# Performance work log

Measured on AMD Instinct MI355X. Metric: run time of the kernel, lower is better.

The kernel has to match this reference:

```python
import jax, jax.numpy as jnp
import numpy as np

EMBED_DIM = 1024
N_HEADS = 16

def setup_inputs() -> dict:
    key = jax.random.key(0)
    k1, k2, k3 = jax.random.split(key, 3)
    x = jax.random.normal(k1, (4, 2048, EMBED_DIM), dtype=jnp.float32)
    # nn.Linear(D, 3D): store weight as [D, 3D] for x @ W
    W_qkv = jax.random.normal(k2, (EMBED_DIM, 3 * EMBED_DIM), dtype=jnp.float32) * (1.0 / np.sqrt(EMBED_DIM))
    b_qkv = jax.random.normal(k3, (3 * EMBED_DIM,), dtype=jnp.float32) * 0.02
    return {"x": x, "W_qkv": W_qkv, "b_qkv": b_qkv}

def reference(x, W_qkv, b_qkv):
    bs, T, D = x.shape
    nh = N_HEADS
    hs = D // nh
    # fused qkv projection -> [bs, T, nh, 3, hs] (matches view(bs,T,nh,3*hs) + split(hs))
    qkv = (jnp.einsum('btd,de->bte', x, W_qkv) + b_qkv).reshape(bs, T, nh, 3, hs)
    q = qkv[..., 0, :].transpose(0, 2, 1, 3)  # [bs, nh, T, hs]
    k = qkv[..., 1, :].transpose(0, 2, 1, 3)
    v = qkv[..., 2, :].transpose(0, 2, 1, 3)
    scale = 1.0 / np.sqrt(hs).astype(np.float32)
    scores = jnp.einsum('bhqd,bhkd->bhqk', q, k) * scale  # [bs, nh, T, T]
    attn = jax.nn.softmax(scores, axis=-1)
    out = jnp.einsum('bhqk,bhkd->bhqd', attn, v)  # [bs, nh, T, hs]
    return out.transpose(0, 2, 1, 3).reshape(bs, T, D)
```

## Files before the change

kernel.cpp:

```cpp
#include <hip/hip_runtime.h>
#include <stdint.h>

#define T_SEQ 2048
#define DMODEL 1024
#define NHEAD 16
#define HS 64
#define N3 3072
#define BSZ 4
#define MTOT (BSZ*T_SEQ)

typedef __attribute__((ext_vector_type(8))) short bf16x8;
typedef __attribute__((ext_vector_type(4))) float f32x4;
typedef __attribute__((ext_vector_type(16))) float f32x16;
typedef __attribute__((ext_vector_type(2))) unsigned int uint2v;

#define QSCALE 0.18033688011112042f
#define SM_SHIFT 12.0f

#define BH_STRIDE 131072

__device__ inline unsigned short f2bf(float f){
  union { float f; uint32_t u; } v; v.f = f;
  uint32_t r = (v.u + 0x7fffu + ((v.u >> 16) & 1u)) >> 16;
  return (unsigned short)r;
}

__device__ inline uint32_t cvtpk_bf16(float lo, float hi){
  uint32_t r;
  asm("v_cvt_pk_bf16_f32 %0, %1, %2" : "=v"(r) : "v"(lo), "v"(hi));
  return r;
}

__device__ inline void plswap(uint32_t &a, uint32_t &b){
  uint2v r = __builtin_amdgcn_permlane32_swap(a, b, false, false);
  a = r[0]; b = r[1];
}

__device__ inline void gld16(const void* g, void* l){
  __builtin_amdgcn_global_load_lds((const __attribute__((address_space(1))) void*)g,
                                   (__attribute__((address_space(3))) void*)l, 16, 0, 0);
}

__global__ __launch_bounds__(256) void cvt_x(const float* __restrict__ x,
                                             unsigned short* __restrict__ xb, int n){
  int stride = gridDim.x * blockDim.x;
  for (int i = blockIdx.x * blockDim.x + threadIdx.x; i * 4 < n; i += stride){
    const float4 v = *(const float4*)(x + (size_t)i * 4);
    ushort4 o; o.x = f2bf(v.x); o.y = f2bf(v.y); o.z = f2bf(v.z); o.w = f2bf(v.w);
    *(ushort4*)(xb + (size_t)i * 4) = o;
  }
}

__global__ __launch_bounds__(256) void cvt_wt(const float* __restrict__ W,
                                              unsigned short* __restrict__ Wt){
  __shared__ float tile[32][33];
  int bx = blockIdx.x;
  int by = blockIdx.y;
  int tx = threadIdx.x;
  int ty = threadIdx.y;
#pragma unroll
  for (int i = 0; i < 4; i++){
    int k = by * 32 + ty + i * 8;
    int n = bx * 32 + tx;
    tile[ty + i * 8][tx] = W[(size_t)k * N3 + n];
  }
  __syncthreads();
#pragma unroll
  for (int i = 0; i < 4; i++){
    int n = bx * 32 + ty + i * 8;
    int k = by * 32 + tx;
    Wt[(size_t)n * DMODEL + k] = f2bf(tile[tx][ty + i * 8]);
  }
}

#define BM 128
#define BN 128
#define BK 32

__global__ __launch_bounds__(256, 2) void gemm_qkv(
    const unsigned short* __restrict__ xb, const unsigned short* __restrict__ wt,
    const float* __restrict__ bias,
    unsigned short* __restrict__ Qb, unsigned short* __restrict__ Kb,
    unsigned short* __restrict__ Vt)
{
  __shared__ unsigned short Al[BM * BK];
  __shared__ unsigned short Bl[BN * BK];
  const int tid = threadIdx.x;
  const int lane = tid & 63;
  const int w  = tid >> 6;
  const int wm = w >> 1, wn = w & 1;
  const int lr = lane & 15, lg = lane >> 4;
  const int m0 = blockIdx.x * BM;
  const int n0 = blockIdx.y * BN;

  f32x4 acc[4][4] = {};

  const int srow = tid >> 2;
  const int scol = (tid & 3) * 8;
  const unsigned short* ga0 = xb + (size_t)(m0 + srow) * DMODEL + scol;
  const unsigned short* gb0 = wt + (size_t)(n0 + srow) * DMODEL + scol;
  unsigned short* la = &Al[tid * 8];
  unsigned short* lb = &Bl[tid * 8];

  for (int k0 = 0; k0 < DMODEL; k0 += BK){
    gld16(ga0 + k0, la);
    gld16(ga0 + k0 + (size_t)64 * DMODEL, la + 2048);
    gld16(gb0 + k0, lb);
    gld16(gb0 + k0 + (size_t)64 * DMODEL, lb + 2048);
    __syncthreads();
    bf16x8 af[4], bfg[4];
#pragma unroll
    for (int i = 0; i < 4; i++){
      af[i]  = *(const bf16x8*)&Al[(wm * 64 + i * 16 + lr) * BK + lg * 8];
      bfg[i] = *(const bf16x8*)&Bl[(wn * 64 + i * 16 + lr) * BK + lg * 8];
    }
#pragma unroll
    for (int i = 0; i < 4; i++)
#pragma unroll
      for (int j = 0; j < 4; j++)
        acc[i][j] = __builtin_amdgcn_mfma_f32_16x16x32_bf16(af[i], bfg[j], acc[i][j], 0, 0, 0);
    __syncthreads();
  }

#pragma unroll
  for (int i = 0; i < 4; i++){
#pragma unroll
    for (int j = 0; j < 4; j++){
      int gn = n0 + wn * 64 + j * 16 + lr;
      float bv = bias[gn];
      int h = gn / 192;
      int rem = gn - h * 192;
      int which = rem >> 6;
      int d = rem & 63;
#pragma unroll
      for (int r = 0; r < 4; r++){
        int gm = m0 + wm * 64 + i * 16 + lg * 4 + r;
        int b = gm >> 11, t = gm & 2047;
        float val = acc[i][j][r] + bv;
        size_t base = (size_t)(b * NHEAD + h) * BH_STRIDE + (size_t)(t >> 5) * 2048;
        if (which == 0)
          Qb[base + (d >> 4) * 512 + ((d >> 3) & 1) * 256 + (t & 31) * 8 + (d & 7)] = f2bf(val * QSCALE);
        else if (which == 1)
          Kb[base + (d >> 4) * 512 + ((d >> 3) & 1) * 256 + (t & 31) * 8 + (d & 7)] = f2bf(val);
        else {
          int kv = t & 31;
          Vt[base + (d >> 5) * 1024 + (kv >> 4) * 512 + ((kv >> 3) & 1) * 256 + (d & 31) * 8 + (kv & 7)] = f2bf(val);
        }
      }
    }
  }
}

__global__ __launch_bounds__(256, 3) void attn(
    const unsigned short* __restrict__ Qb, const unsigned short* __restrict__ Kb,
    const unsigned short* __restrict__ Vt, float* __restrict__ out)
{
  __shared__ unsigned short KVs[2][2][2][2048];

  int flat = blockIdx.x + (blockIdx.y << 4) + (blockIdx.z << 8);
  int wid = (flat & 7) * 128 + (flat >> 3);
  const int bx = wid & 15;
  const int h  = (wid >> 4) & 15;
  const int b  = wid >> 8;

  const int tid = threadIdx.x;
  const int lane = tid & 63;
  const int w = tid >> 6;
  const int ql = lane & 31;
  const int hi = lane >> 5;
  const int bh = b * NHEAD + h;
  const int q0 = bx * 128 + w * 32;

  const unsigned short* Qf = Qb + (size_t)bh * BH_STRIDE;
  const unsigned short* Kg = Kb + (size_t)bh * BH_STRIDE;
  const unsigned short* Vg = Vt + (size_t)bh * BH_STRIDE;

  bf16x8 qf[4];
#pragma unroll
  for (int c = 0; c < 4; c++)
    qf[c] = *(const bf16x8*)(Qf + (size_t)(q0 >> 5) * 2048 + c * 512 + lane * 8);

  f32x16 cinit;
#pragma unroll
  for (int r = 0; r < 16; r++) cinit[r] = -SM_SHIFT;

  f32x16 acc0 = {}, acc1 = {};
  float lA = 0.f, lB = 0.f, lC = 0.f, lD = 0.f;

  gld16(Kg +        tid * 8, &KVs[0][0][0][tid * 8]);
  gld16(Kg + 2048 + tid * 8, &KVs[0][0][1][tid * 8]);
  gld16(Vg +        tid * 8, &KVs[0][1][0][tid * 8]);
  gld16(Vg + 2048 + tid * 8, &KVs[0][1][1][tid * 8]);
  __syncthreads();

#define SOFTMAX_PACK(S, PF1, PF2) \
    uint32_t c8[8]; \
    _Pragma("unroll") \
    for (int i = 0; i < 8; i += 2){ \
      float p0 = __builtin_amdgcn_exp2f((S)[2 * i]); \
      float p1 = __builtin_amdgcn_exp2f((S)[2 * i + 1]); \
      float p2 = __builtin_amdgcn_exp2f((S)[2 * i + 2]); \
      float p3 = __builtin_amdgcn_exp2f((S)[2 * i + 3]); \
      lA += p0; lB += p1; lC += p2; lD += p3; \
      c8[i]     = cvtpk_bf16(p0, p1); \
      c8[i + 1] = cvtpk_bf16(p2, p3); \
    } \
    plswap(c8[0], c8[2]); plswap(c8[1], c8[3]); \
    plswap(c8[4], c8[6]); plswap(c8[5], c8[7]); \
    PF1.u[0] = c8[0]; PF1.u[1] = c8[1]; PF1.u[2] = c8[2]; PF1.u[3] = c8[3]; \
    PF2.u[0] = c8[4]; PF2.u[1] = c8[5]; PF2.u[2] = c8[6]; PF2.u[3] = c8[7];

  for (int t = 0; t < 32; ++t){
    const int cur = t & 1;
    if (t < 31){
      const size_t g0 = (size_t)(2 * t + 2) * 2048 + tid * 8;
      gld16(Kg + g0,        &KVs[cur ^ 1][0][0][tid * 8]);
      gld16(Kg + g0 + 2048, &KVs[cur ^ 1][0][1][tid * 8]);
      gld16(Vg + g0,        &KVs[cur ^ 1][1][0][tid * 8]);
      gld16(Vg + g0 + 2048, &KVs[cur ^ 1][1][1][tid * 8]);
    }

    f32x16 sA;
    {
      bf16x8 kf[4];
#pragma unroll
      for (int c = 0; c < 4; c++) kf[c] = *(const bf16x8*)&KVs[cur][0][0][c * 512 + lane * 8];
      __builtin_amdgcn_s_setprio(1);
      sA = __builtin_amdgcn_mfma_f32_32x32x16_bf16(kf[0], qf[0], cinit, 0, 0, 0);
      sA = __builtin_amdgcn_mfma_f32_32x32x16_bf16(kf[1], qf[1], sA, 0, 0, 0);
      sA = __builtin_amdgcn_mfma_f32_32x32x16_bf16(kf[2], qf[2], sA, 0, 0, 0);
      sA = __builtin_amdgcn_mfma_f32_32x32x16_bf16(kf[3], qf[3], sA, 0, 0, 0);
      __builtin_amdgcn_s_setprio(0);
    }
    f32x16 sB;
    {
      bf16x8 kf[4];
#pragma unroll
      for (int c = 0; c < 4; c++) kf[c] = *(const bf16x8*)&KVs[cur][0][1][c * 512 + lane * 8];
      __builtin_amdgcn_s_setprio(1);
      sB = __builtin_amdgcn_mfma_f32_32x32x16_bf16(kf[0], qf[0], cinit, 0, 0, 0);
      sB = __builtin_amdgcn_mfma_f32_32x32x16_bf16(kf[1], qf[1], sB, 0, 0, 0);
      sB = __builtin_amdgcn_mfma_f32_32x32x16_bf16(kf[2], qf[2], sB, 0, 0, 0);
      sB = __builtin_amdgcn_mfma_f32_32x32x16_bf16(kf[3], qf[3], sB, 0, 0, 0);
      __builtin_amdgcn_s_setprio(0);
    }

    {
      union { uint32_t u[4]; bf16x8 v; } pf1, pf2;
      SOFTMAX_PACK(sA, pf1, pf2)
      bf16x8 vf[4];
#pragma unroll
      for (int c = 0; c < 4; c++) vf[c] = *(const bf16x8*)&KVs[cur][1][0][c * 512 + lane * 8];
      __builtin_amdgcn_s_setprio(1);
      acc0 = __builtin_amdgcn_mfma_f32_32x32x16_bf16(vf[0], pf1.v, acc0, 0, 0, 0);
      acc0 = __builtin_amdgcn_mfma_f32_32x32x16_bf16(vf[1], pf2.v, acc0, 0, 0, 0);
      acc1 = __builtin_amdgcn_mfma_f32_32x32x16_bf16(vf[2], pf1.v, acc1, 0, 0, 0);
      acc1 = __builtin_amdgcn_mfma_f32_32x32x16_bf16(vf[3], pf2.v, acc1, 0, 0, 0);
      __builtin_amdgcn_s_setprio(0);
    }
    {
      union { uint32_t u[4]; bf16x8 v; } pf1, pf2;
      SOFTMAX_PACK(sB, pf1, pf2)
      bf16x8 vf[4];
#pragma unroll
      for (int c = 0; c < 4; c++) vf[c] = *(const bf16x8*)&KVs[cur][1][1][c * 512 + lane * 8];
      __builtin_amdgcn_s_setprio(1);
      acc0 = __builtin_amdgcn_mfma_f32_32x32x16_bf16(vf[0], pf1.v, acc0, 0, 0, 0);
      acc0 = __builtin_amdgcn_mfma_f32_32x32x16_bf16(vf[1], pf2.v, acc0, 0, 0, 0);
      acc1 = __builtin_amdgcn_mfma_f32_32x32x16_bf16(vf[2], pf1.v, acc1, 0, 0, 0);
      acc1 = __builtin_amdgcn_mfma_f32_32x32x16_bf16(vf[3], pf2.v, acc1, 0, 0, 0);
      __builtin_amdgcn_s_setprio(0);
    }

    __syncthreads();
  }
#undef SOFTMAX_PACK

  float l_ = (lA + lB) + (lC + lD);
  l_ += __shfl_xor(l_, 32);
  float inv = 1.0f / l_;

  float* tl = (float*)&KVs[0][0][0][0];
  float* tw = tl + w * (32 * 33);
#pragma unroll
  for (int t2 = 0; t2 < 2; t2++){
    const f32x16& A = t2 ? acc1 : acc0;
#pragma unroll
    for (int r = 0; r < 16; r++){
      int dp = (r & 3) + 8 * (r >> 2) + 4 * hi;
      tw[dp * 33 + ql] = A[r] * inv;
    }
    asm volatile("s_waitcnt lgkmcnt(0)" ::: "memory");
    const int cq = lane >> 3;
    const int cc = (lane & 7) * 4;
#pragma unroll
    for (int it = 0; it < 4; it++){
      int q = it * 8 + cq;
      float4 o;
      o.x = tw[(cc + 0) * 33 + q];
      o.y = tw[(cc + 1) * 33 + q];
      o.z = tw[(cc + 2) * 33 + q];
      o.w = tw[(cc + 3) * 33 + q];
      *(float4*)(out + ((size_t)(b * T_SEQ + q0 + q)) * DMODEL + h * HS + t2 * 32 + cc) = o;
    }
    asm volatile("s_waitcnt lgkmcnt(0)" ::: "memory");
  }
}

extern "C" void kernel_launch(void* const* d_in, const int* in_sizes, int n_in,
                              void* d_out, int out_size, void* d_ws, size_t ws_size,
                              hipStream_t stream) {
  const float* x  = (const float*)d_in[0];
  const float* Wq = (const float*)d_in[1];
  const float* bq = (const float*)d_in[2];
  float* out = (float*)d_out;
  uint8_t* ws = (uint8_t*)d_ws;

  unsigned short* xb = (unsigned short*)(ws);
  unsigned short* wt = (unsigned short*)(ws + (size_t)16 * 1024 * 1024);
  unsigned short* Qb = (unsigned short*)(ws + (size_t)22 * 1024 * 1024);
  unsigned short* Kb = (unsigned short*)(ws + (size_t)38 * 1024 * 1024);
  unsigned short* Vt = (unsigned short*)(ws + (size_t)54 * 1024 * 1024);

  cvt_x<<<2048, 256, 0, stream>>>(x, xb, MTOT * DMODEL);
  cvt_wt<<<dim3(N3 / 32, DMODEL / 32), dim3(32, 8), 0, stream>>>(Wq, wt);
  gemm_qkv<<<dim3(MTOT / BM, N3 / BN), 256, 0, stream>>>(xb, wt, bq, Qb, Kb, Vt);
  attn<<<dim3(T_SEQ / 128, NHEAD, BSZ), 256, 0, stream>>>(Qb, Kb, Vt, out);
}
```

Baseline: 170.0 us.

## Triple-buffer QKV GEMM with larger tiles, swizzled LDS and block remapping

The QKV projection GEMM moves from a single-buffered 128x128x32 tile with 256 threads to a 256x128x64 tile with 512 threads and a three-stage LDS ring. Global-to-LDS loads for tile t+2 are issued between fragment reads and MFMA phases, gated by explicit vmcnt waits and raw barriers, so load latency hides behind compute. LDS columns are XOR-swizzled to avoid bank conflicts. Blocks are remapped for better L2 locality, and MFMA sections run at raised priority. The larger LDS footprint (about 147KB) limits occupancy to one block per CU, and the hand-tuned waitcnt and barrier scheme is fragile.

```diff
diff --git a/kernel.cpp b/kernel.cpp
--- a/kernel.cpp
+++ b/kernel.cpp
@@ -73,54 +73,107 @@
   }
 }
 
-#define BM 128
-#define BN 128
-#define BK 32
-
-__global__ __launch_bounds__(256, 2) void gemm_qkv(
+#define GBM 256
+#define GBN 128
+#define GBK 64
+
+__global__ __launch_bounds__(512, 2) void gemm_qkv(
     const unsigned short* __restrict__ xb, const unsigned short* __restrict__ wt,
     const float* __restrict__ bias,
     unsigned short* __restrict__ Qb, unsigned short* __restrict__ Kb,
     unsigned short* __restrict__ Vt)
 {
-  __shared__ unsigned short Al[BM * BK];
-  __shared__ unsigned short Bl[BN * BK];
+  __shared__ unsigned short Ab[3][GBM * GBK];
+  __shared__ unsigned short Bb[3][GBN * GBK];
+
   const int tid = threadIdx.x;
   const int lane = tid & 63;
-  const int w  = tid >> 6;
-  const int wm = w >> 1, wn = w & 1;
+  const int w = tid >> 6;
+  const int wm = w >> 1;
+  const int wn = w & 1;
   const int lr = lane & 15, lg = lane >> 4;
-  const int m0 = blockIdx.x * BM;
-  const int n0 = blockIdx.y * BN;
+  const int r7 = lr & 7;
+
+  int flat = blockIdx.x + (blockIdx.y << 5);
+  int orig = (flat & 7) * 96 + (flat >> 3);
+  const int mt = orig & 31, nt = orig >> 5;
+  const int m0 = mt * GBM, n0 = nt * GBN;
+
+  const int srow = tid >> 3;
+  const int ks = tid & 7;
+  const int kog = ks ^ (srow & 7);
+  const unsigned short* gaBase = xb + (size_t)(m0 + srow) * DMODEL + kog * 8;
+  const unsigned short* gbBase = wt + (size_t)(n0 + srow) * DMODEL + kog * 8;
+
+#define STAGEA(TT, U, BUF) gld16(gaBase + (size_t)(U) * 65536 + (TT) * 64, &Ab[BUF][(U) * 4096 + tid * 8]);
+#define STAGEB(TT, V, BUF) gld16(gbBase + (size_t)(V) * 65536 + (TT) * 64, &Bb[BUF][(V) * 4096 + tid * 8]);
 
   f32x4 acc[4][4] = {};
 
-  const int srow = tid >> 2;
-  const int scol = (tid & 3) * 8;
-  const unsigned short* ga0 = xb + (size_t)(m0 + srow) * DMODEL + scol;
-  const unsigned short* gb0 = wt + (size_t)(n0 + srow) * DMODEL + scol;
-  unsigned short* la = &Al[tid * 8];
-  unsigned short* lb = &Bl[tid * 8];
-
-  for (int k0 = 0; k0 < DMODEL; k0 += BK){
-    gld16(ga0 + k0, la);
-    gld16(ga0 + k0 + (size_t)64 * DMODEL, la + 2048);
-    gld16(gb0 + k0, lb);
-    gld16(gb0 + k0 + (size_t)64 * DMODEL, lb + 2048);
-    __syncthreads();
-    bf16x8 af[4], bfg[4];
-#pragma unroll
-    for (int i = 0; i < 4; i++){
-      af[i]  = *(const bf16x8*)&Al[(wm * 64 + i * 16 + lr) * BK + lg * 8];
-      bfg[i] = *(const bf16x8*)&Bl[(wn * 64 + i * 16 + lr) * BK + lg * 8];
-    }
-#pragma unroll
-    for (int i = 0; i < 4; i++)
-#pragma unroll
-      for (int j = 0; j < 4; j++)
-        acc[i][j] = __builtin_amdgcn_mfma_f32_16x16x32_bf16(af[i], bfg[j], acc[i][j], 0, 0, 0);
-    __syncthreads();
-  }
+#pragma unroll
+  for (int u = 0; u < 4; u++) STAGEA(0, u, 0)
+  STAGEB(0, 0, 0) STAGEB(0, 1, 0)
+#pragma unroll
+  for (int u = 0; u < 4; u++) STAGEA(1, u, 1)
+  STAGEB(1, 0, 1) STAGEB(1, 1, 1)
+
+  for (int t = 0; t < 16; ++t){
+    const int cb = t % 3;
+    const int sb = (t + 2) % 3;
+    const int ts = (t + 2 <= 15) ? (t + 2) : 15;
+
+    asm volatile("s_waitcnt vmcnt(6)" ::: "memory");
+    __builtin_amdgcn_s_barrier();
+
+    bf16x8 af[4][2], bfr[4][2];
+#pragma unroll
+    for (int fm = 0; fm < 2; fm++)
+#pragma unroll
+      for (int kh = 0; kh < 2; kh++){
+        int row = wm * 64 + fm * 16 + lr;
+        af[fm][kh] = *(const bf16x8*)&Ab[cb][row * 64 + (((kh * 4 + lg) ^ r7)) * 8];
+      }
+#pragma unroll
+    for (int fn = 0; fn < 4; fn++)
+#pragma unroll
+      for (int kh = 0; kh < 2; kh++){
+        int row = wn * 64 + fn * 16 + lr;
+        bfr[fn][kh] = *(const bf16x8*)&Bb[cb][row * 64 + (((kh * 4 + lg) ^ r7)) * 8];
+      }
+    STAGEA(ts, 0, sb) STAGEA(ts, 1, sb) STAGEA(ts, 2, sb)
+    __builtin_amdgcn_s_barrier();
+    __builtin_amdgcn_s_setprio(1);
+#pragma unroll
+    for (int fm = 0; fm < 2; fm++)
+#pragma unroll
+      for (int fn = 0; fn < 4; fn++)
+#pragma unroll
+        for (int kh = 0; kh < 2; kh++)
+          acc[fm][fn] = __builtin_amdgcn_mfma_f32_16x16x32_bf16(af[fm][kh], bfr[fn][kh], acc[fm][fn], 0, 0, 0);
+    __builtin_amdgcn_s_setprio(0);
+    __builtin_amdgcn_s_barrier();
+
+#pragma unroll
+    for (int fm = 2; fm < 4; fm++)
+#pragma unroll
+      for (int kh = 0; kh < 2; kh++){
+        int row = wm * 64 + fm * 16 + lr;
+        af[fm][kh] = *(const bf16x8*)&Ab[cb][row * 64 + (((kh * 4 + lg) ^ r7)) * 8];
+      }
+    STAGEA(ts, 3, sb) STAGEB(ts, 0, sb) STAGEB(ts, 1, sb)
+    __builtin_amdgcn_s_barrier();
+    __builtin_amdgcn_s_setprio(1);
+#pragma unroll
+    for (int fm = 2; fm < 4; fm++)
+#pragma unroll
+      for (int fn = 0; fn < 4; fn++)
+#pragma unroll
+        for (int kh = 0; kh < 2; kh++)
+          acc[fm][fn] = __builtin_amdgcn_mfma_f32_16x16x32_bf16(af[fm][kh], bfr[fn][kh], acc[fm][fn], 0, 0, 0);
+    __builtin_amdgcn_s_setprio(0);
+  }
+#undef STAGEA
+#undef STAGEB
 
 #pragma unroll
   for (int i = 0; i < 4; i++){
@@ -324,6 +377,6 @@
 
   cvt_x<<<2048, 256, 0, stream>>>(x, xb, MTOT * DMODEL);
   cvt_wt<<<dim3(N3 / 32, DMODEL / 32), dim3(32, 8), 0, stream>>>(Wq, wt);
-  gemm_qkv<<<dim3(MTOT / BM, N3 / BN), 256, 0, stream>>>(xb, wt, bq, Qb, Kb, Vt);
+  gemm_qkv<<<dim3(MTOT / GBM, N3 / GBN), 512, 0, stream>>>(xb, wt, bq, Qb, Kb, Vt);
   attn<<<dim3(T_SEQ / 128, NHEAD, BSZ), 256, 0, stream>>>(Qb, Kb, Vt, out);
 }
```

New measurement: 179.6 us. 5.6% more time.
